# Kernel tuning notes

Hardware: AMD Instinct MI355X
Metric: run time of the kernel (lower is better)

## Reference

```python
import jax, jax.numpy as jnp
import numpy as np

NUM_CLASSES = 10
SOFT_CENTER_RADIUS = 3.0
TOPK = 13
IOU_WEIGHT = 3.0
EPS = 1e-07
INF = 100000000.0


def setup_inputs() -> dict:
    key = jax.random.key(0)
    ks = jax.random.split(key, 8)
    B, N, G, C = 8, 16384, 64, NUM_CLASSES
    # priors: [N,4] = (cx, cy, stride_x, stride_y)
    centers = jax.random.uniform(ks[0], (N, 2), minval=0.0, maxval=640.0)
    strides = jnp.full((N, 2), 16.0, dtype=jnp.float32)
    priors = jnp.concatenate([centers, strides], axis=-1)
    # 2D gt boxes (x1,y1,x2,y2) inside a 640px image
    xy = jax.random.uniform(ks[1], (B, G, 2), minval=0.0, maxval=520.0)
    wh = jax.random.uniform(ks[2], (B, G, 2), minval=20.0, maxval=120.0)
    gt_bboxes = jnp.concatenate([xy, xy + wh], axis=-1)
    gt_center = xy + 0.5 * wh
    # 3D boxes: only columns [0,2] (x,z) are used by the dist iou branch
    gt_bboxes_3d = jax.random.normal(ks[3], (B, G, 7)) * 2.0
    pred_bboxes = jax.random.normal(ks[4], (B, N, 7)) * 2.0
    pred_scores = jax.random.normal(ks[5], (B, N, C))
    gt_labels = jax.random.randint(ks[6], (B, G, 1), 0, C, dtype=jnp.int32)
    pad_bbox_flag = jnp.ones((B, G, 1), dtype=jnp.float32)
    return dict(pred_bboxes=pred_bboxes, pred_scores=pred_scores, priors=priors,
                gt_labels=gt_labels, gt_bboxes=gt_bboxes, gt_center=gt_center,
                gt_bboxes_3d=gt_bboxes_3d, pad_bbox_flag=pad_bbox_flag)


def reference(pred_bboxes, pred_scores, priors, gt_labels, gt_bboxes, gt_center,
              gt_bboxes_3d, pad_bbox_flag):
    B, N, _ = pred_bboxes.shape
    G = gt_bboxes.shape[1]

    pc = priors[:, :2]                                   # [N,2]
    # find_inside_points: prior center strictly inside 2D gt box -> [B,N,G]
    cx, cy = pc[None, :, None, 0], pc[None, :, None, 1]
    inside = ((cx > gt_bboxes[:, None, :, 0]) & (cy > gt_bboxes[:, None, :, 1]) &
              (cx < gt_bboxes[:, None, :, 2]) & (cy < gt_bboxes[:, None, :, 3]))
    is_in_gts = inside.astype(jnp.float32) * pad_bbox_flag[:, None, :, 0]  # [B,N,G]
    mask = is_in_gts > 0

    # soft center prior
    strides = priors[None, :, None, 2:]                  # [1,N,1,2]
    diff = (pc[None, :, None, :] - gt_center[:, None, :, :]) / strides
    distance = jnp.linalg.norm(diff, axis=-1) * is_in_gts
    soft_center_prior = 10.0 ** (distance - SOFT_CENTER_RADIUS)

    # dist-type pairwise iou on (x,z) plane
    xz = jnp.array([0, 2])
    pxz = pred_bboxes[:, :, xz]                          # [B,N,2]
    gxz = gt_bboxes_3d[:, :, xz]                         # [B,G,2]
    d = jnp.linalg.norm(pxz[:, :, None, :] - gxz[:, None, :, :], axis=-1)
    pairwise_ious = jnp.clip(1.0 - d / 4.0, 0.0, 1.0)    # [B,N,G]

    iou_cost = -jnp.log(pairwise_ious + EPS) * IOU_WEIGHT

    labels = gt_labels[..., 0]                           # [B,G]
    idx = jnp.broadcast_to(labels[:, None, :], (B, N, G))
    pscores = jnp.take_along_axis(pred_scores, idx, axis=2)  # [B,N,G] logits
    scale = pairwise_ious - jax.nn.sigmoid(pscores)
    # stable BCE-with-logits(pscores, target=pairwise_ious)
    bce = jnp.maximum(pscores, 0.0) - pscores * pairwise_ious + jnp.log1p(jnp.exp(-jnp.abs(pscores)))
    cls_cost = bce * scale ** 2

    cost = jnp.where(mask, cls_cost + iou_cost + soft_center_prior, INF)

    # ---- dynamic k matching ----
    k = min(TOPK, N)
    topk_ious = jax.lax.top_k(jnp.swapaxes(pairwise_ious, 1, 2), k)[0]  # [B,G,k]
    dynamic_ks = jnp.clip(topk_ious.sum(-1).astype(jnp.int32), 1, None)  # [B,G]
    sorted_cost = jnp.sort(cost, axis=1)
    cost_k = jnp.take_along_axis(sorted_cost, dynamic_ks[:, None, :], axis=1)
    cost_k_1 = jnp.take_along_axis(sorted_cost, (dynamic_ks - 1)[:, None, :], axis=1)
    thr = 0.5 * (cost_k + cost_k_1) * is_in_gts          # [B,N,G]
    matching = cost <= thr                               # bool [B,N,G]
    masked_cost = jnp.where(matching, cost, INF)
    multi = matching.sum(-1) > 1                         # prior matched to >1 gt
    argmin_gt = jnp.argmin(masked_cost, axis=2)
    onehot = jax.nn.one_hot(argmin_gt, G, dtype=jnp.bool_)
    matching = jnp.where(multi[..., None], onehot, matching)

    # ---- assemble outputs (dense, jit-friendly version of nonzero indices) ----
    max_index = jnp.argmin(cost, axis=2)                 # [B,N]
    assign_metrics = jnp.take_along_axis(pairwise_ious, max_index[..., None], axis=2)[..., 0]
    matched = matching.any(-1)                           # [B,N]
    gt_idx = jnp.argmax(matching, axis=-1)               # [B,N]
    matched_iou = jnp.take_along_axis(pairwise_ious, gt_idx[..., None], axis=2)[..., 0]
    assign_metrics = jnp.where(matched, matched_iou, assign_metrics)

    assigned_labels = jnp.take_along_axis(labels, max_index, axis=1)  # [B,N]
    assigned_labels = jnp.where(assign_metrics < 1e-07, NUM_CLASSES, assigned_labels)
    assigned_labels = jnp.where(matched, jnp.take_along_axis(labels, gt_idx, axis=1), assigned_labels)

    assigned_labels_weights = jnp.ones((B, N), dtype=jnp.float32)
    return assigned_labels, assigned_labels_weights, assign_metrics, matching
```

## Files before the change

### kernel.cpp

```cpp
#include <hip/hip_runtime.h>
#include <hip/hip_bf16.h>
#include <stdint.h>

#define NCLS 10
#define B_ 8
#define N_ 16384
#define G_ 64
#define INF_ 1.0e8f

typedef unsigned long long u64;
typedef unsigned int u32;

__device__ __forceinline__ u32 ordf(float f) {
    u32 b = __float_as_uint(f);
    return (b & 0x80000000u) ? ~b : (b | 0x80000000u);
}
__device__ __forceinline__ float unordf(u32 u) {
    u32 b = (u & 0x80000000u) ? (u ^ 0x80000000u) : ~u;
    return __uint_as_float(b);
}

__device__ __forceinline__ float iou_pair(float px, float pz, float g3x, float g3z) {
#pragma clang fp contract(off)
    float ddx = px - g3x;
    float ddz = pz - g3z;
    float d = sqrtf(ddx * ddx + ddz * ddz);
    float iou = 1.0f - d / 4.0f;
    return fminf(fmaxf(iou, 0.0f), 1.0f);
}

__device__ __forceinline__ float cost_pair(float cx, float cy, float sx, float sy,
                                           float ps, float gcx, float gcy,
                                           float pad, float iou) {
#pragma clang fp contract(off)
    float dx = (cx - gcx) / sx;
    float dy = (cy - gcy) / sy;
    float dist = sqrtf(dx * dx + dy * dy) * pad;
    float soft = exp10f(dist - 3.0f);
    float iou_cost = -logf(iou + 1e-7f) * 3.0f;
    float e = expf(-fabsf(ps));
    float sig = (ps >= 0.0f) ? (1.0f / (1.0f + e)) : (e / (1.0f + e));
    float scale = iou - sig;
    float bce = fmaxf(ps, 0.0f) - ps * iou + log1pf(e);
    float cls = bce * (scale * scale);
    return cls + iou_cost + soft;
}

__device__ __forceinline__ u32 wave_max_u32(u32 k) {
#pragma unroll
    for (int off = 32; off >= 1; off >>= 1) {
        u32 o = __shfl_xor(k, off, 64);
        k = (o > k) ? o : k;
    }
    return k;
}
__device__ __forceinline__ u32 wave_min_u32(u32 k) {
#pragma unroll
    for (int off = 32; off >= 1; off >>= 1) {
        u32 o = __shfl_xor(k, off, 64);
        k = (o < k) ? o : k;
    }
    return k;
}

__global__ __launch_bounds__(256) void kP(
    const float* __restrict__ priors,
    const float* __restrict__ gt_bboxes,
    const float* __restrict__ pad_flag,
    const float* __restrict__ pred_bboxes,
    u64* __restrict__ mask64,
    u64* __restrict__ bitmapT,
    float2* __restrict__ pxz)
{
    int tid = threadIdx.x;
    int lane = tid & 63;
    if (blockIdx.x < 512) {
        int q = blockIdx.x;
        int b = q >> 6;
        int n = ((q & 63) << 8) | tid;
        u32 wword = ((q & 63) << 2) | (u32)(tid >> 6);
        float4 pr = ((const float4*)priors)[n];
        float cx = pr.x, cy = pr.y;
        u64 m = 0;
        for (int g = 0; g < G_; ++g) {
            int gi = b * G_ + g;
            float4 gbb = ((const float4*)gt_bboxes)[gi];
            float padv = pad_flag[gi];
            bool isin = (cx > gbb.x) && (cy > gbb.y) && (cx < gbb.z) && (cy < gbb.w)
                        && (padv > 0.0f);
            m |= ((u64)isin) << g;
            u64 bal = __ballot(isin);
            if (lane == 0) bitmapT[(((size_t)gi) << 8) | wword] = bal;
        }
        mask64[(size_t)b * N_ + n] = m;
    } else {
        int base = (int)(blockIdx.x - 512) * 2048 + tid;
#pragma unroll
        for (int i = 0; i < 8; ++i) {
            int idx = base + i * 256;
            float2 v;
            v.x = pred_bboxes[(size_t)idx * 7 + 0];
            v.y = pred_bboxes[(size_t)idx * 7 + 2];
            pxz[idx] = v;
        }
    }
}

__global__ __launch_bounds__(256) void k1b(
    const float2* __restrict__ pxz,
    const float* __restrict__ gt_b3d,
    float* __restrict__ iou13)
{
    int wid = ((int)blockIdx.x << 2) | (threadIdx.x >> 6);
    int lane = threadIdx.x & 63;
    int b = wid >> 10;
    int g = (wid >> 4) & 63;
    int chunk = wid & 15;
    int gi = b * G_ + g;
    float g3x = gt_b3d[gi * 7 + 0];
    float g3z = gt_b3d[gi * 7 + 2];
    const float2* pp = pxz + (size_t)b * N_;

    float s[16];
    int n0 = chunk * 1024 + lane;
#pragma unroll
    for (int it = 0; it < 16; ++it) {
        float2 v = pp[n0 + it * 64];
        s[it] = iou_pair(v.x, v.y, g3x, g3z);
    }
#pragma unroll
    for (int p = 1; p < 16; p <<= 1) {
#pragma unroll
        for (int k = p; k >= 1; k >>= 1) {
#pragma unroll
            for (int j = k % p; j <= 15 - k; j += 2 * k) {
#pragma unroll
                for (int i = 0; i < k; ++i) {
                    if (i + j + k <= 15) {
                        if ((i + j) / (2 * p) == (i + j + k) / (2 * p)) {
                            float hi = fmaxf(s[i + j], s[i + j + k]);
                            float lo = fminf(s[i + j], s[i + j + k]);
                            s[i + j] = hi; s[i + j + k] = lo;
                        }
                    }
                }
            }
        }
    }
    float keepv = 0.0f;
    for (int r = 0; r < 13; ++r) {
        u32 mykey = ordf(s[0]);
        u32 m = wave_max_u32(mykey);
        if (lane == r) keepv = unordf(m);
        int winner = __ffsll(__ballot(mykey == m)) - 1;
        if (lane == winner) {
#pragma unroll
            for (int j = 0; j < 13; ++j) s[j] = s[j + 1];
        }
    }
    if (lane < 13) iou13[(size_t)gi * 208 + chunk * 13 + lane] = keepv;
}

__global__ __launch_bounds__(64) void k1c(
    const float* __restrict__ iou13,
    const u64*   __restrict__ bitmapT,
    const float* __restrict__ priors,
    const float2* __restrict__ pxz,
    const float* __restrict__ pred_scores,
    const int*   __restrict__ gt_labels,
    const float* __restrict__ gt_center,
    const float* __restrict__ gt_b3d,
    const float* __restrict__ pad_flag,
    float* __restrict__ thr_half)
{
    int gi = blockIdx.x;
    int lane = threadIdx.x;
    int b = gi >> 6;

    const float* base = iou13 + (size_t)gi * 208;
    float v0 = base[lane];
    float v1 = base[64 + lane];
    float v2 = base[128 + lane];
    float v3 = (lane < 16) ? base[192 + lane] : -3.0e38f;
    { float h = fmaxf(v0, v1), l = fminf(v0, v1); v0 = h; v1 = l; }
    { float h = fmaxf(v2, v3), l = fminf(v2, v3); v2 = h; v3 = l; }
    { float h = fmaxf(v0, v2), l = fminf(v0, v2); v0 = h; v2 = l; }
    { float h = fmaxf(v1, v3), l = fminf(v1, v3); v1 = h; v3 = l; }
    { float h = fmaxf(v1, v2), l = fminf(v1, v2); v1 = h; v2 = l; }
    float sum13 = 0.0f;
    for (int r = 0; r < 13; ++r) {
        u32 mykey = ordf(v0);
        u32 m = wave_max_u32(mykey);
        sum13 += unordf(m);
        int winner = __ffsll(__ballot(mykey == m)) - 1;
        if (lane == winner) { v0 = v1; v1 = v2; v2 = v3; v3 = -3.0e38f; }
    }
    int ks = (int)sum13;
    if (ks < 1) ks = 1;

    float gcx = gt_center[gi * 2 + 0], gcy = gt_center[gi * 2 + 1];
    float g3x = gt_b3d[gi * 7 + 0],   g3z = gt_b3d[gi * 7 + 2];
    float padv = pad_flag[gi];
    int lab = gt_labels[gi];
    const float2* pp = pxz + (size_t)b * N_;
    const float* sc = pred_scores + (size_t)b * N_ * 10;

    float l[14];
#pragma unroll
    for (int j = 0; j < 14; ++j) l[j] = INF_;
#pragma unroll
    for (int j = 0; j < 4; ++j) {
        u32 w = (u32)(lane + 64 * j);
        u64 wv = bitmapT[(((size_t)gi) << 8) | w];
        u32 nb = w << 6;
        while (wv) {
            int bit = __ffsll(wv) - 1;
            wv &= wv - 1;
            int n = (int)(nb | (u32)bit);
            float4 pr = ((const float4*)priors)[n];
            float2 v = pp[n];
            float ps = sc[n * 10 + lab];
            float iou = iou_pair(v.x, v.y, g3x, g3z);
            float cst = cost_pair(pr.x, pr.y, pr.z, pr.w, ps, gcx, gcy, padv, iou);
            if (cst < l[13]) {
                float vv = cst;
#pragma unroll
                for (int jj = 0; jj < 14; ++jj) {
                    float o = l[jj]; bool lt = vv < o;
                    float mn = lt ? vv : o; vv = lt ? o : vv; l[jj] = mn;
                }
            }
        }
    }
    float ck = INF_, ckm1 = INF_;
    for (int r = 0; r < 14; ++r) {
        u32 mykey = ordf(l[0]);
        u32 m = wave_min_u32(mykey);
        float vm = unordf(m);
        if (r == ks - 1) ckm1 = vm;
        if (r == ks)     ck = vm;
        int winner = __ffsll(__ballot(mykey == m)) - 1;
        if (lane == winner) {
#pragma unroll
            for (int j = 0; j < 13; ++j) l[j] = l[j + 1];
            l[13] = INF_;
        }
    }
    if (lane == 0) thr_half[gi] = 0.5f * (ck + ckm1);
}

__global__ __launch_bounds__(256) void k2(
    const float* __restrict__ priors,
    const float2* __restrict__ pxz,
    const float* __restrict__ pred_scores,
    const int*   __restrict__ gt_labels,
    const float* __restrict__ gt_center,
    const float* __restrict__ gt_b3d,
    const float* __restrict__ pad_flag,
    const float* __restrict__ thr_half,
    const u64*   __restrict__ mask64,
    float* __restrict__ out)
{
    __shared__ float s_gcx[G_], s_gcy[G_], s_g3x[G_], s_g3z[G_];
    __shared__ float s_pad[G_], s_thr[G_];
    __shared__ int   s_lab[G_];
    __shared__ u64   s_words[256];

    int b = blockIdx.x >> 6;
    int n0b = (blockIdx.x & 63) << 8;
    int n = n0b | threadIdx.x;
    size_t t = (size_t)b * N_ + n;

    if (threadIdx.x < G_) {
        int gi = b * G_ + threadIdx.x;
        s_gcx[threadIdx.x] = gt_center[gi * 2 + 0];
        s_gcy[threadIdx.x] = gt_center[gi * 2 + 1];
        s_g3x[threadIdx.x] = gt_b3d[gi * 7 + 0];
        s_g3z[threadIdx.x] = gt_b3d[gi * 7 + 2];
        s_pad[threadIdx.x] = pad_flag[gi];
        s_thr[threadIdx.x] = thr_half[gi];
        s_lab[threadIdx.x] = gt_labels[gi];
    }
    __syncthreads();

    const float* sc = pred_scores + (size_t)b * N_ * 10;
    float4 pr = ((const float4*)priors)[n];
    float2 v2p = pxz[(size_t)b * N_ + n];
    float px = v2p.x;
    float pz = v2p.y;

    float iouC = iou_pair(px, pz, s_g3x[0], s_g3z[0]);
    float costC = INF_;
    int   labC = s_lab[0];

    float iouM = 0.0f, costM = 3.0e38f;
    int   labM = 0, argM = 0;
    u64 mmatch = 0;

    u64 m = mask64[t];
    while (m) {
        int g = __ffsll(m) - 1;
        m &= m - 1;
        float gcx = s_gcx[g], gcy = s_gcy[g];
        float g3x = s_g3x[g], g3z = s_g3z[g];
        float padg = s_pad[g];
        int   labg = s_lab[g];
        float th = s_thr[g];
        float ps = sc[n * 10 + labg];
        float iou = iou_pair(px, pz, g3x, g3z);
        float c = cost_pair(pr.x, pr.y, pr.z, pr.w, ps, gcx, gcy, padg, iou);
        if (c < costC) { costC = c; iouC = iou; labC = labg; }
        if (c <= th * padg) {
            mmatch |= 1ull << g;
            if (c < costM) { costM = c; iouM = iou; labM = labg; argM = g; }
        }
    }
    int cm = __popcll(mmatch);
    bool matched = cm > 0;
    u64 outm = (cm > 1) ? (1ull << argM) : mmatch;
    float metric = matched ? iouM : iouC;
    float olab = matched ? (float)labM
                         : ((iouC < 1e-7f) ? (float)NCLS : (float)labC);

    float* out_lab = out;
    float* out_w   = out + (size_t)B_ * N_;
    float* out_met = out + (size_t)2 * B_ * N_;
    float* out_mat = out + (size_t)3 * B_ * N_;
    out_lab[t] = olab;
    out_w[t]   = 1.0f;
    out_met[t] = metric;
    s_words[threadIdx.x] = outm;
    __syncthreads();

    int q  = threadIdx.x & 3;
    int r0 = threadIdx.x >> 2;
    size_t rowbase = (size_t)b * N_ + n0b;
#pragma unroll
    for (int it = 0; it < 4; ++it) {
        int row = r0 + (it << 6);
        u64 wv = s_words[row];
        u32 bits = (u32)(wv >> (q * 16)) & 0xffffu;
        float* dst = out_mat + (rowbase + row) * 64 + q * 16;
#pragma unroll
        for (int jj = 0; jj < 4; ++jj) {
            float4 f;
            f.x = (bits >> (jj * 4 + 0)) & 1u ? 1.0f : 0.0f;
            f.y = (bits >> (jj * 4 + 1)) & 1u ? 1.0f : 0.0f;
            f.z = (bits >> (jj * 4 + 2)) & 1u ? 1.0f : 0.0f;
            f.w = (bits >> (jj * 4 + 3)) & 1u ? 1.0f : 0.0f;
            ((float4*)dst)[jj] = f;
        }
    }
}

extern "C" void kernel_launch(void* const* d_in, const int* in_sizes, int n_in,
                              void* d_out, int out_size, void* d_ws, size_t ws_size,
                              hipStream_t stream)
{
    const float* pred_bboxes = (const float*)d_in[0];
    const float* pred_scores = (const float*)d_in[1];
    const float* priors      = (const float*)d_in[2];
    const int*   gt_labels   = (const int*)d_in[3];
    const float* gt_bboxes   = (const float*)d_in[4];
    const float* gt_center   = (const float*)d_in[5];
    const float* gt_b3d      = (const float*)d_in[6];
    const float* pad_flag    = (const float*)d_in[7];
    float* out = (float*)d_out;

    char* ws = (char*)d_ws;
    u64* mask64   = (u64*)ws;
    u64* bitmapT  = (u64*)(ws + 1048576);
    float2* pxz   = (float2*)(ws + 2097152);
    float* iou13  = (float*)(ws + 3145728);
    float* thr_half = (float*)(ws + 3145728 + 425984);

    kP<<<576, 256, 0, stream>>>(priors, gt_bboxes, pad_flag, pred_bboxes,
                                mask64, bitmapT, pxz);
    k1b<<<2048, 256, 0, stream>>>(pxz, gt_b3d, iou13);
    k1c<<<512, 64, 0, stream>>>(iou13, bitmapT, priors, pxz,
                                pred_scores, gt_labels, gt_center, gt_b3d,
                                pad_flag, thr_half);
    k2<<<512, 256, 0, stream>>>(priors, pxz, pred_scores, gt_labels,
                                gt_center, gt_b3d, pad_flag,
                                thr_half, mask64, out);
}
```

Measured before the change: 85.72 us.

## Halve per-wave chunk in top-k IoU pass and split candidate scan across four waves

k1b now gives each wave 512 priors (8 per lane) instead of 1024, using a fixed 8-element sorting network and branchless shifting, which doubles the grid and trims register pressure. k1c moves from one wave to four per gt: each wave reduces a quarter of the IoU partial top-13 lists and a quarter of the inside-bitmap words, and wave 0 then merges the results through shared memory to compute dynamic k and the cost threshold. The intent is more parallelism and shorter serial chains in the small-grid stages. The cost is a larger workspace and an extra block barrier plus merge step.

Measured after the change: 82.65 us. 3.6% less time.

```diff
diff --git a/kernel.cpp b/kernel.cpp
--- a/kernel.cpp
+++ b/kernel.cpp
@@ -106,6 +106,8 @@
     }
 }
 
+#define CSWAPD(a, b) { float _h = fmaxf(a, b), _l = fminf(a, b); a = _h; b = _l; }
+
 __global__ __launch_bounds__(256) void k1b(
     const float2* __restrict__ pxz,
     const float* __restrict__ gt_b3d,
@@ -113,55 +115,52 @@
 {
     int wid = ((int)blockIdx.x << 2) | (threadIdx.x >> 6);
     int lane = threadIdx.x & 63;
-    int b = wid >> 10;
-    int g = (wid >> 4) & 63;
-    int chunk = wid & 15;
+    int b = wid >> 11;
+    int g = (wid >> 5) & 63;
+    int chunk = wid & 31;
     int gi = b * G_ + g;
     float g3x = gt_b3d[gi * 7 + 0];
     float g3z = gt_b3d[gi * 7 + 2];
-    const float2* pp = pxz + (size_t)b * N_;
-
-    float s[16];
-    int n0 = chunk * 1024 + lane;
-#pragma unroll
-    for (int it = 0; it < 16; ++it) {
-        float2 v = pp[n0 + it * 64];
-        s[it] = iou_pair(v.x, v.y, g3x, g3z);
-    }
-#pragma unroll
-    for (int p = 1; p < 16; p <<= 1) {
-#pragma unroll
-        for (int k = p; k >= 1; k >>= 1) {
-#pragma unroll
-            for (int j = k % p; j <= 15 - k; j += 2 * k) {
-#pragma unroll
-                for (int i = 0; i < k; ++i) {
-                    if (i + j + k <= 15) {
-                        if ((i + j) / (2 * p) == (i + j + k) / (2 * p)) {
-                            float hi = fmaxf(s[i + j], s[i + j + k]);
-                            float lo = fminf(s[i + j], s[i + j + k]);
-                            s[i + j] = hi; s[i + j + k] = lo;
-                        }
-                    }
-                }
-            }
-        }
-    }
+    const float2* pp = pxz + (size_t)b * N_ + (size_t)(chunk * 512 + lane);
+
+    float2 e0 = pp[0],   e1 = pp[64],  e2 = pp[128], e3 = pp[192];
+    float2 e4 = pp[256], e5 = pp[320], e6 = pp[384], e7 = pp[448];
+    float s0 = iou_pair(e0.x, e0.y, g3x, g3z);
+    float s1 = iou_pair(e1.x, e1.y, g3x, g3z);
+    float s2 = iou_pair(e2.x, e2.y, g3x, g3z);
+    float s3 = iou_pair(e3.x, e3.y, g3x, g3z);
+    float s4 = iou_pair(e4.x, e4.y, g3x, g3z);
+    float s5 = iou_pair(e5.x, e5.y, g3x, g3z);
+    float s6 = iou_pair(e6.x, e6.y, g3x, g3z);
+    float s7 = iou_pair(e7.x, e7.y, g3x, g3z);
+
+    CSWAPD(s0, s1) CSWAPD(s2, s3) CSWAPD(s4, s5) CSWAPD(s6, s7)
+    CSWAPD(s0, s2) CSWAPD(s1, s3) CSWAPD(s4, s6) CSWAPD(s5, s7)
+    CSWAPD(s1, s2) CSWAPD(s5, s6)
+    CSWAPD(s0, s4) CSWAPD(s1, s5) CSWAPD(s2, s6) CSWAPD(s3, s7)
+    CSWAPD(s2, s4) CSWAPD(s3, s5)
+    CSWAPD(s1, s2) CSWAPD(s3, s4) CSWAPD(s5, s6)
+
     float keepv = 0.0f;
     for (int r = 0; r < 13; ++r) {
-        u32 mykey = ordf(s[0]);
+        u32 mykey = ordf(s0);
         u32 m = wave_max_u32(mykey);
         if (lane == r) keepv = unordf(m);
         int winner = __ffsll(__ballot(mykey == m)) - 1;
-        if (lane == winner) {
-#pragma unroll
-            for (int j = 0; j < 13; ++j) s[j] = s[j + 1];
-        }
-    }
-    if (lane < 13) iou13[(size_t)gi * 208 + chunk * 13 + lane] = keepv;
-}
-
-__global__ __launch_bounds__(64) void k1c(
+        bool win = (lane == winner);
+        s0 = win ? s1 : s0;
+        s1 = win ? s2 : s1;
+        s2 = win ? s3 : s2;
+        s3 = win ? s4 : s3;
+        s4 = win ? s5 : s4;
+        s5 = win ? s6 : s5;
+        s6 = win ? s7 : s6;
+        s7 = win ? -3.0e38f : s7;
+    }
+    if (lane < 13) iou13[(size_t)gi * 416 + chunk * 13 + lane] = keepv;
+}
+
+__global__ __launch_bounds__(256) void k1c(
     const float* __restrict__ iou13,
     const u64*   __restrict__ bitmapT,
     const float* __restrict__ priors,
@@ -173,30 +172,28 @@
     const float* __restrict__ pad_flag,
     float* __restrict__ thr_half)
 {
+    __shared__ float s_i[4 * 13];
+    __shared__ float s_c[4 * 14];
     int gi = blockIdx.x;
-    int lane = threadIdx.x;
     int b = gi >> 6;
-
-    const float* base = iou13 + (size_t)gi * 208;
+    int lane = threadIdx.x & 63;
+    int w = threadIdx.x >> 6;
+
+    const float* base = iou13 + (size_t)gi * 416 + w * 104;
     float v0 = base[lane];
-    float v1 = base[64 + lane];
-    float v2 = base[128 + lane];
-    float v3 = (lane < 16) ? base[192 + lane] : -3.0e38f;
-    { float h = fmaxf(v0, v1), l = fminf(v0, v1); v0 = h; v1 = l; }
-    { float h = fmaxf(v2, v3), l = fminf(v2, v3); v2 = h; v3 = l; }
-    { float h = fmaxf(v0, v2), l = fminf(v0, v2); v0 = h; v2 = l; }
-    { float h = fmaxf(v1, v3), l = fminf(v1, v3); v1 = h; v3 = l; }
-    { float h = fmaxf(v1, v2), l = fminf(v1, v2); v1 = h; v2 = l; }
-    float sum13 = 0.0f;
-    for (int r = 0; r < 13; ++r) {
-        u32 mykey = ordf(v0);
-        u32 m = wave_max_u32(mykey);
-        sum13 += unordf(m);
-        int winner = __ffsll(__ballot(mykey == m)) - 1;
-        if (lane == winner) { v0 = v1; v1 = v2; v2 = v3; v3 = -3.0e38f; }
-    }
-    int ks = (int)sum13;
-    if (ks < 1) ks = 1;
+    float v1 = (lane < 40) ? base[64 + lane] : -3.0e38f;
+    if (v1 > v0) { float t = v0; v0 = v1; v1 = t; }
+    {
+        float keepv = 0.0f;
+        for (int r = 0; r < 13; ++r) {
+            u32 mykey = ordf(v0);
+            u32 m = wave_max_u32(mykey);
+            if (lane == r) keepv = unordf(m);
+            int winner = __ffsll(__ballot(mykey == m)) - 1;
+            if (lane == winner) { v0 = v1; v1 = -3.0e38f; }
+        }
+        if (lane < 13) s_i[w * 13 + lane] = keepv;
+    }
 
     float gcx = gt_center[gi * 2 + 0], gcy = gt_center[gi * 2 + 1];
     float g3x = gt_b3d[gi * 7 + 0],   g3z = gt_b3d[gi * 7 + 2];
@@ -208,11 +205,10 @@
     float l[14];
 #pragma unroll
     for (int j = 0; j < 14; ++j) l[j] = INF_;
-#pragma unroll
-    for (int j = 0; j < 4; ++j) {
-        u32 w = (u32)(lane + 64 * j);
-        u64 wv = bitmapT[(((size_t)gi) << 8) | w];
-        u32 nb = w << 6;
+    {
+        u32 word = (u32)(w * 64 + lane);
+        u64 wv = bitmapT[(((size_t)gi) << 8) | word];
+        u32 nb = word << 6;
         while (wv) {
             int bit = __ffsll(wv) - 1;
             wv &= wv - 1;
@@ -232,21 +228,49 @@
             }
         }
     }
-    float ck = INF_, ckm1 = INF_;
-    for (int r = 0; r < 14; ++r) {
-        u32 mykey = ordf(l[0]);
-        u32 m = wave_min_u32(mykey);
-        float vm = unordf(m);
-        if (r == ks - 1) ckm1 = vm;
-        if (r == ks)     ck = vm;
-        int winner = __ffsll(__ballot(mykey == m)) - 1;
-        if (lane == winner) {
-#pragma unroll
-            for (int j = 0; j < 13; ++j) l[j] = l[j + 1];
-            l[13] = INF_;
-        }
-    }
-    if (lane == 0) thr_half[gi] = 0.5f * (ck + ckm1);
+    {
+        float keepc = 0.0f;
+        for (int r = 0; r < 14; ++r) {
+            u32 mykey = ordf(l[0]);
+            u32 m = wave_min_u32(mykey);
+            if (lane == r) keepc = unordf(m);
+            int winner = __ffsll(__ballot(mykey == m)) - 1;
+            if (lane == winner) {
+#pragma unroll
+                for (int j = 0; j < 13; ++j) l[j] = l[j + 1];
+                l[13] = 3.0e38f;
+            }
+        }
+        if (lane < 14) s_c[w * 14 + lane] = keepc;
+    }
+    __syncthreads();
+
+    if (w == 0) {
+        float vi = (lane < 52) ? s_i[lane] : -3.0e38f;
+        float sum13 = 0.0f;
+        for (int r = 0; r < 13; ++r) {
+            u32 mykey = ordf(vi);
+            u32 m = wave_max_u32(mykey);
+            sum13 += unordf(m);
+            int winner = __ffsll(__ballot(mykey == m)) - 1;
+            if (lane == winner) vi = -3.0e38f;
+        }
+        int ks = (int)sum13;
+        if (ks < 1) ks = 1;
+
+        float vc = (lane < 56) ? s_c[lane] : 3.0e38f;
+        float ck = INF_, ckm1 = INF_;
+        for (int r = 0; r < 14; ++r) {
+            u32 mykey = ordf(vc);
+            u32 m = wave_min_u32(mykey);
+            float vm = unordf(m);
+            if (r == ks - 1) ckm1 = vm;
+            if (r == ks)     ck = vm;
+            int winner = __ffsll(__ballot(mykey == m)) - 1;
+            if (lane == winner) vc = 3.0e38f;
+        }
+        if (lane == 0) thr_half[gi] = 0.5f * (ck + ckm1);
+    }
 }
 
 __global__ __launch_bounds__(256) void k2(
@@ -372,14 +396,14 @@
     u64* bitmapT  = (u64*)(ws + 1048576);
     float2* pxz   = (float2*)(ws + 2097152);
     float* iou13  = (float*)(ws + 3145728);
-    float* thr_half = (float*)(ws + 3145728 + 425984);
+    float* thr_half = (float*)(ws + 3145728 + 851968);
 
     kP<<<576, 256, 0, stream>>>(priors, gt_bboxes, pad_flag, pred_bboxes,
                                 mask64, bitmapT, pxz);
-    k1b<<<2048, 256, 0, stream>>>(pxz, gt_b3d, iou13);
-    k1c<<<512, 64, 0, stream>>>(iou13, bitmapT, priors, pxz,
-                                pred_scores, gt_labels, gt_center, gt_b3d,
-                                pad_flag, thr_half);
+    k1b<<<4096, 256, 0, stream>>>(pxz, gt_b3d, iou13);
+    k1c<<<512, 256, 0, stream>>>(iou13, bitmapT, priors, pxz,
+                                 pred_scores, gt_labels, gt_center, gt_b3d,
+                                 pad_flag, thr_half);
     k2<<<512, 256, 0, stream>>>(priors, pxz, pred_scores, gt_labels,
                                 gt_center, gt_b3d, pad_flag,
                                 thr_half, mask64, out);
```
